# Optimization experiments

Measured on AMD Instinct MI355X. Metric: run time of the kernel, lower is better.

The kernel has to match this reference:

```python
import jax, jax.numpy as jnp
import numpy as np


def dct_matrix(N):
    # Orthonormal DCT-II matrix: 2D DCT (scipy fftpack dct ortho applied on both axes) = M @ X @ M.T
    n = jnp.arange(N, dtype=jnp.float32)
    M = jnp.cos(jnp.pi * (2.0 * n[None, :] + 1.0) * n[:, None] / (2.0 * N)) * jnp.sqrt(2.0 / N)
    M = M.at[0].multiply(1.0 / jnp.sqrt(2.0))
    return M


def setup_inputs() -> dict:
    key = jax.random.key(0)
    k1, k2, k3, k4, k5 = jax.random.split(key, 5)
    B, T, C, H, W = 8, 32, 3, 224, 224
    images = jax.random.uniform(k1, (B, T, C, H, W), dtype=jnp.float32)
    w1 = jax.random.normal(k2, (256, 128), dtype=jnp.float32) * 0.05
    b1 = jax.random.normal(k3, (256,), dtype=jnp.float32) * 0.05
    w2 = jax.random.normal(k4, (768, 256), dtype=jnp.float32) * 0.05
    b2 = jax.random.normal(k5, (768,), dtype=jnp.float32) * 0.05
    return {"images": images, "w1": w1, "b1": b1, "w2": w2, "b2": b2}


def reference(images, w1, b1, w2, b2):
    B, T, C, H, W = images.shape
    # (img*255).astype(np.uint8): truncation toward zero (inputs in [0,1) so floor)
    u8 = jnp.floor(jnp.clip(images * 255.0, 0.0, 255.0))
    # cv2.COLOR_RGB2GRAY: Y = 0.299R + 0.587G + 0.114B, rounded to uint8
    gray = jnp.round(0.299 * u8[:, :, 0] + 0.587 * u8[:, :, 1] + 0.114 * u8[:, :, 2])  # [B,T,H,W]
    # Full-frame 2D orthonormal DCT-II via matmul (H == W assumed)
    M = dct_matrix(H)
    dct = jnp.einsum('ih,bthw,jw->btij', M, gray, M)  # [B,T,H,W]
    # Block feature extraction: for each 32-strided block origin, keep dct[i:i+8, j:j+8].flatten()[:16]
    nbi, nbj = H // 32, W // 32
    rows = (jnp.arange(nbi) * 32)[:, None] + jnp.arange(2)   # [nbi,2]
    cols = (jnp.arange(nbj) * 32)[:, None] + jnp.arange(8)   # [nbj,8]
    sub = jnp.take(dct, rows.reshape(-1), axis=2)            # [B,T,nbi*2,W]
    sub = jnp.take(sub, cols.reshape(-1), axis=3)            # [B,T,nbi*2,nbj*8]
    sub = sub.reshape(B, T, nbi, 2, nbj, 8).transpose(0, 1, 2, 4, 3, 5).reshape(B, T, -1)
    feats = sub[:, :, :128].astype(jnp.float32)              # [B,T,128]
    # fc: Linear(128,256) -> ReLU -> Dropout(eval: identity) -> Linear(256, embed_dim)
    h = jax.nn.relu(jnp.einsum('btf,of->bto', feats, w1) + b1)
    return jnp.einsum('bth,oh->bto', h, w2) + b2
```

## Files before the change

### kernel.cpp

```cpp
#include <hip/hip_runtime.h>
#include <math.h>

#define HW 224
#define NCOL 56

__device__ __forceinline__ float dctM(int r, int k) {
    int m = ((2 * k + 1) * r) % (4 * HW);
    float ang = (float)m * (3.14159265358979323846f / (2.0f * HW));
    float v = cosf(ang);
    v *= (r == 0) ? 0.06681531047810609f : 0.09449111825230679f;
    return v;
}

__global__ __launch_bounds__(512) void k1_feats(const float* __restrict__ img,
                                                float* __restrict__ feats) {
    __shared__ float msel[4 * HW];
    __shared__ float mcol[HW * NCOL];
    __shared__ float tpart[2 * 4 * HW];
    __shared__ float tmp[4 * HW];

    const int tid = threadIdx.x;
    const int frame = blockIdx.x;

    for (int idx = tid; idx < 4 * HW; idx += 512) {
        int i = idx / HW, h = idx % HW;
        int r = (i < 2) ? i : (30 + i);
        msel[idx] = dctM(r, h);
    }
    for (int idx = tid; idx < HW * NCOL; idx += 512) {
        int w = idx / NCOL, jj = idx % NCOL;
        int j = ((jj >> 3) << 5) + (jj & 7);
        mcol[idx] = dctM(j, w);
    }
    __syncthreads();

    const int w = tid & 255;
    const int half = tid >> 8;
    if (w < HW) {
        const float* p = img + (size_t)frame * (3 * HW * HW) + half * (112 * HW) + w;
        float a0 = 0.f, a1 = 0.f, a2 = 0.f, a3 = 0.f;
        const int hbase = half * 112;
        #pragma unroll 4
        for (int h = 0; h < 112; ++h) {
            float r = p[h * HW];
            float g = p[HW * HW + h * HW];
            float b = p[2 * HW * HW + h * HW];
            float ru = floorf(fminf(fmaxf(r * 255.f, 0.f), 255.f));
            float gu = floorf(fminf(fmaxf(g * 255.f, 0.f), 255.f));
            float bu = floorf(fminf(fmaxf(b * 255.f, 0.f), 255.f));
            float gray = rintf(0.299f * ru + 0.587f * gu + 0.114f * bu);
            int hh = hbase + h;
            a0 += msel[0 * HW + hh] * gray;
            a1 += msel[1 * HW + hh] * gray;
            a2 += msel[2 * HW + hh] * gray;
            a3 += msel[3 * HW + hh] * gray;
        }
        tpart[(half * 4 + 0) * HW + w] = a0;
        tpart[(half * 4 + 1) * HW + w] = a1;
        tpart[(half * 4 + 2) * HW + w] = a2;
        tpart[(half * 4 + 3) * HW + w] = a3;
    }
    __syncthreads();
    for (int idx = tid; idx < 4 * HW; idx += 512)
        tmp[idx] = tpart[idx] + tpart[4 * HW + idx];
    __syncthreads();

    if (tid < 4 * NCOL) {
        int i = tid / NCOL, jj = tid % NCOL;
        float s = 0.f;
        #pragma unroll 8
        for (int w2 = 0; w2 < HW; ++w2)
            s += tmp[i * HW + w2] * mcol[w2 * NCOL + jj];
        int f = -1;
        if (i < 2) {
            f = (jj >> 3) * 16 + i * 8 + (jj & 7);
        } else if (jj < 8) {
            f = 112 + (i - 2) * 8 + jj;
        }
        if (f >= 0) feats[frame * 128 + f] = s;
    }
}

__global__ __launch_bounds__(256) void k2_fc1(const float* __restrict__ feats,
                                              const float* __restrict__ w1,
                                              const float* __restrict__ b1,
                                              float* __restrict__ hbuf) {
    __shared__ float sA[16 * 129];
    __shared__ float sW[16 * 129];
    const int tid = threadIdx.x;
    const int fg = blockIdx.x, og = blockIdx.y;
    for (int idx = tid; idx < 16 * 128; idx += 256) {
        int r = idx >> 7, c = idx & 127;
        sA[r * 129 + c] = feats[(fg * 16 + r) * 128 + c];
        sW[r * 129 + c] = w1[(og * 16 + r) * 128 + c];
    }
    __syncthreads();
    const int fr = tid >> 4, o = tid & 15;
    float s = 0.f;
    #pragma unroll 8
    for (int f = 0; f < 128; ++f)
        s += sA[fr * 129 + f] * sW[o * 129 + f];
    s += b1[og * 16 + o];
    hbuf[(fg * 16 + fr) * 256 + og * 16 + o] = fmaxf(s, 0.f);
}

__global__ __launch_bounds__(256) void k3_fc2(const float* __restrict__ hbuf,
                                              const float* __restrict__ w2,
                                              const float* __restrict__ b2,
                                              float* __restrict__ out) {
    __shared__ float sH[16 * 257];
    __shared__ float sW[16 * 257];
    const int tid = threadIdx.x;
    const int fg = blockIdx.x, eg = blockIdx.y;
    for (int idx = tid; idx < 16 * 256; idx += 256) {
        int r = idx >> 8, c = idx & 255;
        sH[r * 257 + c] = hbuf[(fg * 16 + r) * 256 + c];
        sW[r * 257 + c] = w2[(eg * 16 + r) * 256 + c];
    }
    __syncthreads();
    const int fr = tid >> 4, e = tid & 15;
    float s = 0.f;
    #pragma unroll 8
    for (int k = 0; k < 256; ++k)
        s += sH[fr * 257 + k] * sW[e * 257 + k];
    s += b2[eg * 16 + e];
    out[(fg * 16 + fr) * 768 + eg * 16 + e] = s;
}

extern "C" void kernel_launch(void* const* d_in, const int* in_sizes, int n_in,
                              void* d_out, int out_size, void* d_ws, size_t ws_size,
                              hipStream_t stream) {
    const float* img = (const float*)d_in[0];
    const float* w1  = (const float*)d_in[1];
    const float* b1  = (const float*)d_in[2];
    const float* w2  = (const float*)d_in[3];
    const float* b2  = (const float*)d_in[4];
    float* out = (float*)d_out;

    float* feats = (float*)d_ws;
    float* hbuf  = feats + 256 * 128;

    k1_feats<<<256, 512, 0, stream>>>(img, feats);
    k2_fc1<<<dim3(16, 16), 256, 0, stream>>>(feats, w1, b1, hbuf);
    k3_fc2<<<dim3(16, 48), 256, 0, stream>>>(hbuf, w2, b2, out);
}
```

Measured before the change: 51.65 us.

## Vectorize image loads with float4 strips and alias shared buffers in DCT kernel

```diff
diff --git a/kernel.cpp b/kernel.cpp
--- a/kernel.cpp
+++ b/kernel.cpp
@@ -12,12 +12,18 @@
     return v;
 }
 
+__device__ __forceinline__ float gray_px(float r, float g, float b) {
+    float ru = floorf(r * 255.f);
+    float gu = floorf(g * 255.f);
+    float bu = floorf(b * 255.f);
+    return rintf(fmaf(0.299f, ru, fmaf(0.587f, gu, 0.114f * bu)));
+}
+
 __global__ __launch_bounds__(512) void k1_feats(const float* __restrict__ img,
                                                 float* __restrict__ feats) {
     __shared__ float msel[4 * HW];
-    __shared__ float mcol[HW * NCOL];
-    __shared__ float tpart[2 * 4 * HW];
     __shared__ float tmp[4 * HW];
+    __shared__ float buf[HW * NCOL];
 
     const int tid = threadIdx.x;
     const int frame = blockIdx.x;
@@ -27,42 +33,53 @@
         int r = (i < 2) ? i : (30 + i);
         msel[idx] = dctM(r, h);
     }
+    __syncthreads();
+
+    const int cg = tid & 63;
+    const int strip = tid >> 6;
+    if (cg < 56) {
+        const float* p = img + (size_t)frame * (3 * HW * HW) + (strip * 28) * HW + cg * 4;
+        float4 a0 = {0, 0, 0, 0}, a1 = {0, 0, 0, 0}, a2 = {0, 0, 0, 0}, a3 = {0, 0, 0, 0};
+        #pragma unroll 4
+        for (int h = 0; h < 28; ++h) {
+            const float4 r4 = *(const float4*)(p + h * HW);
+            const float4 g4 = *(const float4*)(p + HW * HW + h * HW);
+            const float4 b4 = *(const float4*)(p + 2 * HW * HW + h * HW);
+            float gx = gray_px(r4.x, g4.x, b4.x);
+            float gy = gray_px(r4.y, g4.y, b4.y);
+            float gz = gray_px(r4.z, g4.z, b4.z);
+            float gw = gray_px(r4.w, g4.w, b4.w);
+            int hh = strip * 28 + h;
+            float m0 = msel[0 * HW + hh];
+            float m1 = msel[1 * HW + hh];
+            float m2 = msel[2 * HW + hh];
+            float m3 = msel[3 * HW + hh];
+            a0.x += m0 * gx; a0.y += m0 * gy; a0.z += m0 * gz; a0.w += m0 * gw;
+            a1.x += m1 * gx; a1.y += m1 * gy; a1.z += m1 * gz; a1.w += m1 * gw;
+            a2.x += m2 * gx; a2.y += m2 * gy; a2.z += m2 * gz; a2.w += m2 * gw;
+            a3.x += m3 * gx; a3.y += m3 * gy; a3.z += m3 * gz; a3.w += m3 * gw;
+        }
+        float* tp = buf + strip * (4 * HW) + cg * 4;
+        *(float4*)(tp + 0 * HW) = a0;
+        *(float4*)(tp + 1 * HW) = a1;
+        *(float4*)(tp + 2 * HW) = a2;
+        *(float4*)(tp + 3 * HW) = a3;
+    }
+    __syncthreads();
+
+    for (int idx = tid; idx < 4 * HW; idx += 512) {
+        float s = 0.f;
+        #pragma unroll
+        for (int st = 0; st < 8; ++st) s += buf[st * (4 * HW) + idx];
+        tmp[idx] = s;
+    }
+    __syncthreads();
+
     for (int idx = tid; idx < HW * NCOL; idx += 512) {
         int w = idx / NCOL, jj = idx % NCOL;
         int j = ((jj >> 3) << 5) + (jj & 7);
-        mcol[idx] = dctM(j, w);
+        buf[idx] = dctM(j, w);
     }
-    __syncthreads();
-
-    const int w = tid & 255;
-    const int half = tid >> 8;
-    if (w < HW) {
-        const float* p = img + (size_t)frame * (3 * HW * HW) + half * (112 * HW) + w;
-        float a0 = 0.f, a1 = 0.f, a2 = 0.f, a3 = 0.f;
-        const int hbase = half * 112;
-        #pragma unroll 4
-        for (int h = 0; h < 112; ++h) {
-            float r = p[h * HW];
-            float g = p[HW * HW + h * HW];
-            float b = p[2 * HW * HW + h * HW];
-            float ru = floorf(fminf(fmaxf(r * 255.f, 0.f), 255.f));
-            float gu = floorf(fminf(fmaxf(g * 255.f, 0.f), 255.f));
-            float bu = floorf(fminf(fmaxf(b * 255.f, 0.f), 255.f));
-            float gray = rintf(0.299f * ru + 0.587f * gu + 0.114f * bu);
-            int hh = hbase + h;
-            a0 += msel[0 * HW + hh] * gray;
-            a1 += msel[1 * HW + hh] * gray;
-            a2 += msel[2 * HW + hh] * gray;
-            a3 += msel[3 * HW + hh] * gray;
-        }
-        tpart[(half * 4 + 0) * HW + w] = a0;
-        tpart[(half * 4 + 1) * HW + w] = a1;
-        tpart[(half * 4 + 2) * HW + w] = a2;
-        tpart[(half * 4 + 3) * HW + w] = a3;
-    }
-    __syncthreads();
-    for (int idx = tid; idx < 4 * HW; idx += 512)
-        tmp[idx] = tpart[idx] + tpart[4 * HW + idx];
     __syncthreads();
 
     if (tid < 4 * NCOL) {
@@ -70,7 +87,7 @@
         float s = 0.f;
         #pragma unroll 8
         for (int w2 = 0; w2 < HW; ++w2)
-            s += tmp[i * HW + w2] * mcol[w2 * NCOL + jj];
+            s += tmp[i * HW + w2] * buf[w2 * NCOL + jj];
         int f = -1;
         if (i < 2) {
             f = (jj >> 3) * 16 + i * 8 + (jj & 7);
```

Result: no change. 52.00 us (+0.7%).
